# Kernel optimization log

Measured on AMD Instinct MI355X. Metric: run time of the kernel, lower is better.

## Reference

```python
import jax, jax.numpy as jnp
import numpy as np

D = 64          # feature dim
H_POS = 64      # pos_mlp hidden
H_ATTN = 4 * D  # attn_mlp hidden
B, N = 1, 1024


def setup_inputs() -> dict:
    key = jax.random.key(0)
    ks = jax.random.split(key, 12)
    s = lambda fan_in: 1.0 / np.sqrt(fan_in)
    return {
        "x": jax.random.normal(ks[0], (B, N, D), jnp.float32),
        "pos": jax.random.normal(ks[1], (B, N, 2), jnp.float32),
        "Wq": jax.random.normal(ks[2], (D, D), jnp.float32) * s(D),
        "Wk": jax.random.normal(ks[3], (D, D), jnp.float32) * s(D),
        "Wv": jax.random.normal(ks[4], (D, D), jnp.float32) * s(D),
        "pW1": jax.random.normal(ks[5], (2, H_POS), jnp.float32) * s(2),
        "pb1": jnp.zeros((H_POS,), jnp.float32),
        "pW2": jax.random.normal(ks[6], (H_POS, D), jnp.float32) * s(H_POS),
        "pb2": jnp.zeros((D,), jnp.float32),
        "aW1": jax.random.normal(ks[7], (D, H_ATTN), jnp.float32) * s(D),
        "ab1": jnp.zeros((H_ATTN,), jnp.float32),
        "aW2": jax.random.normal(ks[8], (H_ATTN, D), jnp.float32) * s(H_ATTN),
        "ab2": jnp.zeros((D,), jnp.float32),
    }


def reference(x, pos, Wq, Wk, Wv, pW1, pb1, pW2, pb2, aW1, ab1, aW2, ab2):
    # projections: [b, n, d]
    q = x @ Wq
    k = x @ Wk
    v = x @ Wv
    # pairwise relative positions: [b, i, j, 2]
    rel_pos = pos[:, :, None, :] - pos[:, None, :, :]
    # pos MLP: [b, i, j, d]
    rpe = jax.nn.relu(rel_pos @ pW1 + pb1) @ pW2 + pb2
    # pairwise q - k: [b, i, j, d]
    qk_rel = q[:, :, None, :] - k[:, None, :, :]
    # values broadcast over i, plus positional embedding: [b, i, j, d]
    vv = v[:, None, :, :] + rpe
    # attention MLP on (qk_rel + rpe): [b, i, j, d]
    sim = jax.nn.relu((qk_rel + rpe) @ aW1 + ab1) @ aW2 + ab2
    # softmax over j (axis=-2), per-channel
    attn = jax.nn.softmax(sim, axis=-2)
    # weighted aggregation: [b, i, d]
    agg = jnp.einsum('bijd,bijd->bid', attn, vv)
    return agg
```

## Files before the change

### kernel.cpp

```cpp
#include <hip/hip_runtime.h>


typedef float f32x4 __attribute__((ext_vector_type(4)));
typedef int   i32x8 __attribute__((ext_vector_type(8)));
using sh8 = __attribute__((ext_vector_type(8))) short;

static constexpr int NPTS = 1024;

#if __has_builtin(__builtin_amdgcn_exp2f)
#define EXP2(x) __builtin_amdgcn_exp2f(x)
#else
#define EXP2(x) exp2f(x)
#endif

static constexpr size_t BEXT8_OFF = 0;
static constexpr size_t AW2F_OFF = 32768;
static constexpr size_t PW2F_OFF = 49152;
static constexpr size_t CARR_OFF = 57344;
static constexpr size_t AI_OFF   = 58368;
static constexpr size_t VPT_OFF  = 320512;
static constexpr size_t AJ_OFF   = 582656;
static constexpr size_t KN8_OFF  = 713728;
static constexpr size_t QA_OFF   = 779264;

__device__ __forceinline__ unsigned short f2b_rne(float f) {
    unsigned u = __float_as_uint(f);
    u += 0x7fffu + ((u >> 16) & 1u);
    return (unsigned short)(u >> 16);
}
__device__ __forceinline__ unsigned pk2(float lo, float hi) {
    return __builtin_amdgcn_perm(__float_as_uint(hi), __float_as_uint(lo), 0x07060302);
}
__device__ __forceinline__ float b2f(unsigned short s) {
    return __uint_as_float(((unsigned)s) << 16);
}
__device__ __forceinline__ unsigned char f2fp8(float v) {
    return (unsigned char)(__builtin_amdgcn_cvt_pk_fp8_f32(v, 0.f, 0, false) & 0xff);
}
__device__ __forceinline__ unsigned pk4fp8(float a, float b, float c, float d) {
    int r = __builtin_amdgcn_cvt_pk_fp8_f32(a, b, 0, false);
    r = __builtin_amdgcn_cvt_pk_fp8_f32(c, d, r, true);
    return (unsigned)r;
}
__device__ __forceinline__ i32x8 ld32B(const void* p) {
    const uint4 a = ((const uint4*)p)[0];
    const uint4 b = ((const uint4*)p)[1];
    i32x8 r;
    r[0] = a.x; r[1] = a.y; r[2] = a.z; r[3] = a.w;
    r[4] = b.x; r[5] = b.y; r[6] = b.z; r[7] = b.w;
    return r;
}

__global__ void prep_all(const float* __restrict__ x, const float* __restrict__ pos,
                         const float* __restrict__ Wq, const float* __restrict__ Wk,
                         const float* __restrict__ Wv, const float* __restrict__ pW1,
                         const float* __restrict__ pb1, const float* __restrict__ pW2,
                         const float* __restrict__ pb2, const float* __restrict__ aW1,
                         const float* __restrict__ ab1, const float* __restrict__ aW2,
                         unsigned char* __restrict__ bext8, unsigned char* __restrict__ aw2f8,
                         unsigned short* __restrict__ pw2f, float* __restrict__ cArr,
                         unsigned char* __restrict__ kN8, float* __restrict__ vPT,
                         float* __restrict__ aI, unsigned short* __restrict__ aJ,
                         float* __restrict__ qa)
{
    __shared__ float s1[4][64];
    __shared__ float s2[4][64];
    const int b = blockIdx.x;
    if (b < 128) {
        const int r = b * 256 + threadIdx.x;
        const int frag = r >> 11, lane = (r >> 5) & 63, e = r & 31;
        const int w = frag >> 2, nt = frag & 3;
        const int tl = lane & 15, qq = lane >> 4;
        const int k = qq * 32 + e;
        const int t = 64 * w + 16 * nt + tl;
        float val;
        if (k < 64) {
            float s = 0.f;
            for (int d = 0; d < 64; ++d) s = fmaf(pW2[k * 64 + d], aW1[d * 256 + t], s);
            val = s;
        } else {
            val = aW1[(k - 64) * 256 + t];
        }
        bext8[r] = f2fp8(val);
    } else if (b < 192) {
        const int r = (b - 128) * 256 + threadIdx.x;
        const int e = r & 31, lane = (r >> 5) & 63, wsl = (r >> 11) & 3, kb = r >> 13;
        const int q = lane >> 4, dl = lane & 15;
        const int kp = kb * 128 + q * 32 + e;
        const int t = 64 * (kp >> 6) + 16 * (kp & 3) + ((kp >> 2) & 15);
        const int d = 16 * wsl + dl;
        aw2f8[r] = f2fp8(aW2[t * 64 + d] * 1.4426950408889634f);
    } else if (b < 208) {
        const int r = (b - 192) * 256 + threadIdx.x;
        const int k = r >> 6, d = r & 63;
        const int kc = k >> 5, kl = k & 31, qq = kl >> 3, e = kl & 7;
        const int nt = d >> 4, dl = d & 15;
        pw2f[(((size_t)(kc * 4 + nt) * 64) + (qq * 16 + dl)) * 8 + e] = f2b_rne(pW2[k * 64 + d]);
    } else if (b == 208) {
        const int t = threadIdx.x;
        float s = ab1[t];
        for (int d = 0; d < 64; ++d) s = fmaf(pb2[d], aW1[d * 256 + t], s);
        cArr[t] = s;
    } else if (b < 465) {
        const int t = threadIdx.x, sub = t >> 6, d = t & 63;
        const int i = (b - 209) * 4 + sub;
        s1[sub][d] = x[i * 64 + d];
        __syncthreads();
        float k = 0.f, v = 0.f;
        for (int e = 0; e < 64; ++e) {
            const float xe = s1[sub][e];
            k = fmaf(xe, Wk[e * 64 + d], k);
            v = fmaf(xe, Wv[e * 64 + d], v);
        }
        const float a = pos[i * 2] * pW1[d] + pos[i * 2 + 1] * pW1[64 + d];
        kN8[i * 64 + d] = f2fp8(-k);
        vPT[d * NPTS + i] = v + pb2[d];
        aI[i * 64 + d] = a + pb1[d];
        aJ[i * 64 + d] = f2b_rne(a);
    } else {
        const int i = b - 465, t = threadIdx.x;
        if (t < 64) s1[0][t] = x[i * 64 + t];
        __syncthreads();
        if (t < 64) {
            float s = 0.f;
            for (int e = 0; e < 64; ++e) s = fmaf(s1[0][e], Wq[e * 64 + t], s);
            s2[0][t] = s;
        }
        __syncthreads();
        float s = 0.f;
        for (int d = 0; d < 64; ++d) s = fmaf(s2[0][d], aW1[d * 256 + t], s);
        qa[(size_t)i * 256 + t] = s;
    }
}

__global__ __launch_bounds__(256, 2) void ptl_main(
    const float* __restrict__ aI, const unsigned short* __restrict__ aJ,
    const unsigned char* __restrict__ kN8, const float* __restrict__ vPT,
    const unsigned char* __restrict__ bext8, const unsigned char* __restrict__ aw2f8,
    const unsigned short* __restrict__ pw2f, const float* __restrict__ cArr,
    const float* __restrict__ qa, float* __restrict__ out)
{
    const int i    = blockIdx.x;
    const int tid  = threadIdx.x;
    const int w    = tid >> 6;
    const int lane = tid & 63;
    const int m    = lane & 15;
    const int q    = lane >> 4;

    __shared__ __align__(16) uint4 AfL[2][2][2][64];
    __shared__ __align__(16) unsigned char Af8[2][2][16 * 144];
    __shared__ __align__(16) unsigned char Hs[2][2][16 * 272];

    i32x8 B8f[4];
#pragma unroll
    for (int nt = 0; nt < 4; ++nt)
        B8f[nt] = ld32B(bext8 + ((size_t)((4 * w + nt) * 64 + lane)) * 32);
    i32x8 W2f[2];
#pragma unroll
    for (int kb = 0; kb < 2; ++kb)
        W2f[kb] = ld32B(aw2f8 + ((size_t)((kb * 4 + w) * 64 + lane)) * 32);
    sh8 P2f[2];
#pragma unroll
    for (int kc = 0; kc < 2; ++kc)
        P2f[kc] = *(const sh8*)(pw2f + ((size_t)((kc * 4 + w) * 64 + lane)) * 8);

    float creg[4];
#pragma unroll
    for (int nt = 0; nt < 4; ++nt)
        creg[nt] = cArr[64 * w + 16 * nt + m] + qa[(size_t)i * 256 + 64 * w + 16 * nt + m];

    const int s_ = w >> 1, h_ = w & 1;
    const unsigned short* bsrcA  = aJ  + m * 64 + h_ * 32 + q * 8;
    const unsigned char*  bsrcK8 = kN8 + m * 64 + h_ * 32 + q * 8;
    const float*          ibase  = aI + (size_t)i * 64 + h_ * 32 + q * 8;
    float iv[8];
    *(float4*)(iv)     = *(const float4*)(ibase);
    *(float4*)(iv + 4) = *(const float4*)(ibase + 4);

    {
        const sh8  rawA  = *(const sh8*)(bsrcA + (size_t)(16 * s_) * 64);
        const uint2 rawK = *(const uint2*)(bsrcK8 + (size_t)(16 * s_) * 64);
        float t[8];
#pragma unroll
        for (int e = 0; e < 8; ++e)
            t[e] = fmaxf(iv[e] - b2f((unsigned short)rawA[e]), 0.f);
        uint4 pk;
        pk.x = pk2(t[0], t[1]); pk.y = pk2(t[2], t[3]);
        pk.z = pk2(t[4], t[5]); pk.w = pk2(t[6], t[7]);
        AfL[0][s_][h_][lane] = pk;
        uint2 f8;
        f8.x = pk4fp8(t[0], t[1], t[2], t[3]);
        f8.y = pk4fp8(t[4], t[5], t[6], t[7]);
        *(uint2*)(Af8[0][s_] + m * 144 + h_ * 32 + q * 8)      = f8;
        *(uint2*)(Af8[0][s_] + m * 144 + 64 + h_ * 32 + q * 8) = rawK;
    }
    __syncthreads();

    float num = 0.f, den = 0.f;
    const f32x4 z4 = {0.f, 0.f, 0.f, 0.f};
    f32x4 aRp0 = z4, aRp1 = z4;
    const float* vbase = vPT + (size_t)(16 * w + m) * NPTS;

    for (int n = 0; n < 32; ++n) {
        const int pb = n & 1, nb = pb ^ 1;
        const int j0 = n << 5;

        sh8  rawA;
        uint2 rawK;
        if (n < 31) {
            rawA = *(const sh8*)(bsrcA + (size_t)(j0 + 32 + 16 * s_) * 64);
            rawK = *(const uint2*)(bsrcK8 + (size_t)(j0 + 32 + 16 * s_) * 64);
        }
        const float4 vj0 = *(const float4*)(vbase + j0 + 4 * q);
        const float4 vj1 = *(const float4*)(vbase + j0 + 16 + 4 * q);

        {
            const i32x8 A8 = ld32B(Af8[pb][0] + m * 144 + 32 * q);
            f32x4 acc[4];
#pragma unroll
            for (int nt = 0; nt < 4; ++nt) {
                const f32x4 cv = {creg[nt], creg[nt], creg[nt], creg[nt]};
                acc[nt] = __builtin_amdgcn_mfma_scale_f32_16x16x128_f8f6f4(
                    A8, B8f[nt], cv, 0, 0, 0, 127, 0, 127);
            }
            unsigned char* hw = Hs[pb][0] + (4 * q) * 272 + 64 * w + 4 * m;
#pragma unroll
            for (int r = 0; r < 4; ++r)
                *(unsigned*)(hw + r * 272) = pk4fp8(fmaxf(acc[0][r], 0.f), fmaxf(acc[1][r], 0.f),
                                                   fmaxf(acc[2][r], 0.f), fmaxf(acc[3][r], 0.f));
        }

        i32x8 h00, h01, h10, h11;
        if (n) {
            h00 = ld32B(Hs[nb][0] + m * 272 + 0   + 32 * q);
            h01 = ld32B(Hs[nb][0] + m * 272 + 128 + 32 * q);
            h10 = ld32B(Hs[nb][1] + m * 272 + 0   + 32 * q);
            h11 = ld32B(Hs[nb][1] + m * 272 + 128 + 32 * q);
        }

        {
            const i32x8 A8 = ld32B(Af8[pb][1] + m * 144 + 32 * q);
            f32x4 acc[4];
#pragma unroll
            for (int nt = 0; nt < 4; ++nt) {
                const f32x4 cv = {creg[nt], creg[nt], creg[nt], creg[nt]};
                acc[nt] = __builtin_amdgcn_mfma_scale_f32_16x16x128_f8f6f4(
                    A8, B8f[nt], cv, 0, 0, 0, 127, 0, 127);
            }
            unsigned char* hw = Hs[pb][1] + (4 * q) * 272 + 64 * w + 4 * m;
#pragma unroll
            for (int r = 0; r < 4; ++r)
                *(unsigned*)(hw + r * 272) = pk4fp8(fmaxf(acc[0][r], 0.f), fmaxf(acc[1][r], 0.f),
                                                   fmaxf(acc[2][r], 0.f), fmaxf(acc[3][r], 0.f));
        }

        const sh8 A00 = *(const sh8*)&AfL[pb][0][0][lane];
        const sh8 A01 = *(const sh8*)&AfL[pb][0][1][lane];
        const sh8 A10 = *(const sh8*)&AfL[pb][1][0][lane];
        const sh8 A11 = *(const sh8*)&AfL[pb][1][1][lane];

        if (n) {
            f32x4 aS0 = z4, aS1 = z4;
            aS0 = __builtin_amdgcn_mfma_scale_f32_16x16x128_f8f6f4(
                h00, W2f[0], aS0, 0, 0, 0, 127, 0, 127);
            aS0 = __builtin_amdgcn_mfma_scale_f32_16x16x128_f8f6f4(
                h01, W2f[1], aS0, 0, 0, 0, 127, 0, 127);
            aS1 = __builtin_amdgcn_mfma_scale_f32_16x16x128_f8f6f4(
                h10, W2f[0], aS1, 0, 0, 0, 127, 0, 127);
            aS1 = __builtin_amdgcn_mfma_scale_f32_16x16x128_f8f6f4(
                h11, W2f[1], aS1, 0, 0, 0, 127, 0, 127);
#pragma unroll
            for (int r = 0; r < 4; ++r) {
                const float e0 = EXP2(aS0[r]);
                num = fmaf(e0, aRp0[r], num);
                den += e0;
                const float e1 = EXP2(aS1[r]);
                num = fmaf(e1, aRp1[r], num);
                den += e1;
            }
        }

        const f32x4 vc0 = {vj0.x, vj0.y, vj0.z, vj0.w};
        const f32x4 vc1 = {vj1.x, vj1.y, vj1.z, vj1.w};
        f32x4 aR0 = __builtin_amdgcn_mfma_f32_16x16x32_bf16(A00, P2f[0], vc0, 0, 0, 0);
        aR0 = __builtin_amdgcn_mfma_f32_16x16x32_bf16(A01, P2f[1], aR0, 0, 0, 0);
        f32x4 aR1 = __builtin_amdgcn_mfma_f32_16x16x32_bf16(A10, P2f[0], vc1, 0, 0, 0);
        aR1 = __builtin_amdgcn_mfma_f32_16x16x32_bf16(A11, P2f[1], aR1, 0, 0, 0);
        aRp0 = aR0;
        aRp1 = aR1;

        if (n < 31) {
            float t[8];
#pragma unroll
            for (int e = 0; e < 8; ++e)
                t[e] = fmaxf(iv[e] - b2f((unsigned short)rawA[e]), 0.f);
            uint4 pk;
            pk.x = pk2(t[0], t[1]); pk.y = pk2(t[2], t[3]);
            pk.z = pk2(t[4], t[5]); pk.w = pk2(t[6], t[7]);
            AfL[nb][s_][h_][lane] = pk;
            uint2 f8;
            f8.x = pk4fp8(t[0], t[1], t[2], t[3]);
            f8.y = pk4fp8(t[4], t[5], t[6], t[7]);
            *(uint2*)(Af8[nb][s_] + m * 144 + h_ * 32 + q * 8)      = f8;
            *(uint2*)(Af8[nb][s_] + m * 144 + 64 + h_ * 32 + q * 8) = rawK;
        }

        __syncthreads();
    }

    {
        f32x4 aS0 = z4, aS1 = z4;
        const i32x8 h00 = ld32B(Hs[1][0] + m * 272 + 0   + 32 * q);
        const i32x8 h01 = ld32B(Hs[1][0] + m * 272 + 128 + 32 * q);
        const i32x8 h10 = ld32B(Hs[1][1] + m * 272 + 0   + 32 * q);
        const i32x8 h11 = ld32B(Hs[1][1] + m * 272 + 128 + 32 * q);
        aS0 = __builtin_amdgcn_mfma_scale_f32_16x16x128_f8f6f4(
            h00, W2f[0], aS0, 0, 0, 0, 127, 0, 127);
        aS0 = __builtin_amdgcn_mfma_scale_f32_16x16x128_f8f6f4(
            h01, W2f[1], aS0, 0, 0, 0, 127, 0, 127);
        aS1 = __builtin_amdgcn_mfma_scale_f32_16x16x128_f8f6f4(
            h10, W2f[0], aS1, 0, 0, 0, 127, 0, 127);
        aS1 = __builtin_amdgcn_mfma_scale_f32_16x16x128_f8f6f4(
            h11, W2f[1], aS1, 0, 0, 0, 127, 0, 127);
#pragma unroll
        for (int r = 0; r < 4; ++r) {
            const float e0 = EXP2(aS0[r]);
            num = fmaf(e0, aRp0[r], num);
            den += e0;
            const float e1 = EXP2(aS1[r]);
            num = fmaf(e1, aRp1[r], num);
            den += e1;
        }
    }

    num += __shfl_xor(num, 16);
    num += __shfl_xor(num, 32);
    den += __shfl_xor(den, 16);
    den += __shfl_xor(den, 32);
    if (q == 0) out[i * 64 + 16 * w + m] = num / den;
}

extern "C" void kernel_launch(void* const* d_in, const int* in_sizes, int n_in,
                              void* d_out, int out_size, void* d_ws, size_t ws_size,
                              hipStream_t stream) {
    const float* x   = (const float*)d_in[0];
    const float* pos = (const float*)d_in[1];
    const float* Wq  = (const float*)d_in[2];
    const float* Wk  = (const float*)d_in[3];
    const float* Wv  = (const float*)d_in[4];
    const float* pW1 = (const float*)d_in[5];
    const float* pb1 = (const float*)d_in[6];
    const float* pW2 = (const float*)d_in[7];
    const float* pb2 = (const float*)d_in[8];
    const float* aW1 = (const float*)d_in[9];
    const float* ab1 = (const float*)d_in[10];
    const float* aW2 = (const float*)d_in[11];

    char* ws = (char*)d_ws;
    unsigned char*  bext8 = (unsigned char*)(ws + BEXT8_OFF);
    unsigned char*  aw2f8 = (unsigned char*)(ws + AW2F_OFF);
    unsigned short* pw2f  = (unsigned short*)(ws + PW2F_OFF);
    float*          cArr  = (float*)(ws + CARR_OFF);
    float*          aIa   = (float*)(ws + AI_OFF);
    float*          vPTa  = (float*)(ws + VPT_OFF);
    unsigned short* aJa   = (unsigned short*)(ws + AJ_OFF);
    unsigned char*  kN8a  = (unsigned char*)(ws + KN8_OFF);
    float*          qaA   = (float*)(ws + QA_OFF);

    prep_all<<<1489, 256, 0, stream>>>(x, pos, Wq, Wk, Wv, pW1, pb1, pW2, pb2, aW1, ab1, aW2,
                                       bext8, aw2f8, pw2f, cArr, kN8a, vPTa, aIa, aJa, qaA);
    ptl_main<<<NPTS, 256, 0, stream>>>(aIa, aJa, kN8a, vPTa, bext8, aw2f8, pw2f, cArr, qaA,
                                       (float*)d_out);
}
```

Baseline: 159.7 us.

## Process 64 neighbours per pipeline step to halve barrier count

Each loop iteration now handles four 16-row j-slices (64 neighbours) instead of two, so the loop runs 16 times rather than 32. The shared-memory double buffers for A, fp8 A and hidden activations are doubled in size, and each wave builds two slices per step. This halves the number of __syncthreads barriers and gives more independent MFMA work between loads to hide latency. In exchange it raises register and LDS pressure, which could lower occupancy under launch_bounds(256,2).

Result: no change. 162.5 us (+1.7%).

```diff
diff --git a/kernel.cpp b/kernel.cpp
--- a/kernel.cpp
+++ b/kernel.cpp
@@ -147,9 +147,9 @@
     const int m    = lane & 15;
     const int q    = lane >> 4;
 
-    __shared__ __align__(16) uint4 AfL[2][2][2][64];
-    __shared__ __align__(16) unsigned char Af8[2][2][16 * 144];
-    __shared__ __align__(16) unsigned char Hs[2][2][16 * 272];
+    __shared__ __align__(16) uint4 AfL[2][4][2][64];
+    __shared__ __align__(16) unsigned char Af8[2][4][16 * 144];
+    __shared__ __align__(16) unsigned char Hs[2][4][16 * 272];
 
     i32x8 B8f[4];
 #pragma unroll
@@ -169,7 +169,7 @@
     for (int nt = 0; nt < 4; ++nt)
         creg[nt] = cArr[64 * w + 16 * nt + m] + qa[(size_t)i * 256 + 64 * w + 16 * nt + m];
 
-    const int s_ = w >> 1, h_ = w & 1;
+    const int h_ = w & 1, sA = w >> 1;
     const unsigned short* bsrcA  = aJ  + m * 64 + h_ * 32 + q * 8;
     const unsigned char*  bsrcK8 = kN8 + m * 64 + h_ * 32 + q * 8;
     const float*          ibase  = aI + (size_t)i * 64 + h_ * 32 + q * 8;
@@ -177,9 +177,7 @@
     *(float4*)(iv)     = *(const float4*)(ibase);
     *(float4*)(iv + 4) = *(const float4*)(ibase + 4);
 
-    {
-        const sh8  rawA  = *(const sh8*)(bsrcA + (size_t)(16 * s_) * 64);
-        const uint2 rawK = *(const uint2*)(bsrcK8 + (size_t)(16 * s_) * 64);
+    auto build = [&](int buf, int s, const sh8& rawA, const uint2& rawK) {
         float t[8];
 #pragma unroll
         for (int e = 0; e < 8; ++e)
@@ -187,150 +185,152 @@
         uint4 pk;
         pk.x = pk2(t[0], t[1]); pk.y = pk2(t[2], t[3]);
         pk.z = pk2(t[4], t[5]); pk.w = pk2(t[6], t[7]);
-        AfL[0][s_][h_][lane] = pk;
+        AfL[buf][s][h_][lane] = pk;
         uint2 f8;
         f8.x = pk4fp8(t[0], t[1], t[2], t[3]);
         f8.y = pk4fp8(t[4], t[5], t[6], t[7]);
-        *(uint2*)(Af8[0][s_] + m * 144 + h_ * 32 + q * 8)      = f8;
-        *(uint2*)(Af8[0][s_] + m * 144 + 64 + h_ * 32 + q * 8) = rawK;
+        *(uint2*)(Af8[buf][s] + m * 144 + h_ * 32 + q * 8)      = f8;
+        *(uint2*)(Af8[buf][s] + m * 144 + 64 + h_ * 32 + q * 8) = rawK;
+    };
+
+    auto g1pass = [&](int buf, int s) {
+        const i32x8 A8 = ld32B(Af8[buf][s] + m * 144 + 32 * q);
+        f32x4 acc[4];
+#pragma unroll
+        for (int nt = 0; nt < 4; ++nt) {
+            const f32x4 cv = {creg[nt], creg[nt], creg[nt], creg[nt]};
+            acc[nt] = __builtin_amdgcn_mfma_scale_f32_16x16x128_f8f6f4(
+                A8, B8f[nt], cv, 0, 0, 0, 127, 0, 127);
+        }
+        unsigned char* hw = Hs[buf][s] + (4 * q) * 272 + 64 * w + 4 * m;
+#pragma unroll
+        for (int r = 0; r < 4; ++r)
+            *(unsigned*)(hw + r * 272) = pk4fp8(fmaxf(acc[0][r], 0.f), fmaxf(acc[1][r], 0.f),
+                                                fmaxf(acc[2][r], 0.f), fmaxf(acc[3][r], 0.f));
+    };
+
+    {
+        const sh8  rA0 = *(const sh8*)(bsrcA + (size_t)(16 * sA) * 64);
+        const sh8  rA1 = *(const sh8*)(bsrcA + (size_t)(16 * (sA + 2)) * 64);
+        const uint2 rK0 = *(const uint2*)(bsrcK8 + (size_t)(16 * sA) * 64);
+        const uint2 rK1 = *(const uint2*)(bsrcK8 + (size_t)(16 * (sA + 2)) * 64);
+        build(0, sA, rA0, rK0);
+        build(0, sA + 2, rA1, rK1);
     }
     __syncthreads();
 
     float num = 0.f, den = 0.f;
     const f32x4 z4 = {0.f, 0.f, 0.f, 0.f};
-    f32x4 aRp0 = z4, aRp1 = z4;
+    f32x4 aRp0 = z4, aRp1 = z4, aRp2 = z4, aRp3 = z4;
     const float* vbase = vPT + (size_t)(16 * w + m) * NPTS;
 
-    for (int n = 0; n < 32; ++n) {
+    auto g2pair = [&](const i32x8& h00, const i32x8& h01, const i32x8& h10,
+                      const i32x8& h11, const f32x4& p0, const f32x4& p1) {
+        f32x4 aS0 = z4, aS1 = z4;
+        aS0 = __builtin_amdgcn_mfma_scale_f32_16x16x128_f8f6f4(h00, W2f[0], aS0, 0, 0, 0, 127, 0, 127);
+        aS0 = __builtin_amdgcn_mfma_scale_f32_16x16x128_f8f6f4(h01, W2f[1], aS0, 0, 0, 0, 127, 0, 127);
+        aS1 = __builtin_amdgcn_mfma_scale_f32_16x16x128_f8f6f4(h10, W2f[0], aS1, 0, 0, 0, 127, 0, 127);
+        aS1 = __builtin_amdgcn_mfma_scale_f32_16x16x128_f8f6f4(h11, W2f[1], aS1, 0, 0, 0, 127, 0, 127);
+#pragma unroll
+        for (int r = 0; r < 4; ++r) {
+            const float e0 = EXP2(aS0[r]);
+            num = fmaf(e0, p0[r], num);
+            den += e0;
+            const float e1 = EXP2(aS1[r]);
+            num = fmaf(e1, p1[r], num);
+            den += e1;
+        }
+    };
+
+    for (int n = 0; n < 16; ++n) {
         const int pb = n & 1, nb = pb ^ 1;
-        const int j0 = n << 5;
-
-        sh8  rawA;
-        uint2 rawK;
-        if (n < 31) {
-            rawA = *(const sh8*)(bsrcA + (size_t)(j0 + 32 + 16 * s_) * 64);
-            rawK = *(const uint2*)(bsrcK8 + (size_t)(j0 + 32 + 16 * s_) * 64);
+        const int j0 = n << 6;
+
+        sh8  rA0, rA1;
+        uint2 rK0, rK1;
+        if (n < 15) {
+            rA0 = *(const sh8*)(bsrcA + (size_t)(j0 + 64 + 16 * sA) * 64);
+            rA1 = *(const sh8*)(bsrcA + (size_t)(j0 + 64 + 16 * (sA + 2)) * 64);
+            rK0 = *(const uint2*)(bsrcK8 + (size_t)(j0 + 64 + 16 * sA) * 64);
+            rK1 = *(const uint2*)(bsrcK8 + (size_t)(j0 + 64 + 16 * (sA + 2)) * 64);
         }
         const float4 vj0 = *(const float4*)(vbase + j0 + 4 * q);
         const float4 vj1 = *(const float4*)(vbase + j0 + 16 + 4 * q);
+        const float4 vj2 = *(const float4*)(vbase + j0 + 32 + 4 * q);
+        const float4 vj3 = *(const float4*)(vbase + j0 + 48 + 4 * q);
+
+        g1pass(pb, 0);
+        g1pass(pb, 1);
+
+        i32x8 ha0, ha1, hb0, hb1;
+        if (n) {
+            ha0 = ld32B(Hs[nb][0] + m * 272 + 0   + 32 * q);
+            ha1 = ld32B(Hs[nb][0] + m * 272 + 128 + 32 * q);
+            hb0 = ld32B(Hs[nb][1] + m * 272 + 0   + 32 * q);
+            hb1 = ld32B(Hs[nb][1] + m * 272 + 128 + 32 * q);
+        }
+
+        g1pass(pb, 2);
+        g1pass(pb, 3);
+
+        if (n) g2pair(ha0, ha1, hb0, hb1, aRp0, aRp1);
+
+        if (n) {
+            const i32x8 hc0 = ld32B(Hs[nb][2] + m * 272 + 0   + 32 * q);
+            const i32x8 hc1 = ld32B(Hs[nb][2] + m * 272 + 128 + 32 * q);
+            const i32x8 hd0 = ld32B(Hs[nb][3] + m * 272 + 0   + 32 * q);
+            const i32x8 hd1 = ld32B(Hs[nb][3] + m * 272 + 128 + 32 * q);
+            g2pair(hc0, hc1, hd0, hd1, aRp2, aRp3);
+        }
 
         {
-            const i32x8 A8 = ld32B(Af8[pb][0] + m * 144 + 32 * q);
-            f32x4 acc[4];
-#pragma unroll
-            for (int nt = 0; nt < 4; ++nt) {
-                const f32x4 cv = {creg[nt], creg[nt], creg[nt], creg[nt]};
-                acc[nt] = __builtin_amdgcn_mfma_scale_f32_16x16x128_f8f6f4(
-                    A8, B8f[nt], cv, 0, 0, 0, 127, 0, 127);
-            }
-            unsigned char* hw = Hs[pb][0] + (4 * q) * 272 + 64 * w + 4 * m;
-#pragma unroll
-            for (int r = 0; r < 4; ++r)
-                *(unsigned*)(hw + r * 272) = pk4fp8(fmaxf(acc[0][r], 0.f), fmaxf(acc[1][r], 0.f),
-                                                   fmaxf(acc[2][r], 0.f), fmaxf(acc[3][r], 0.f));
-        }
-
-        i32x8 h00, h01, h10, h11;
-        if (n) {
-            h00 = ld32B(Hs[nb][0] + m * 272 + 0   + 32 * q);
-            h01 = ld32B(Hs[nb][0] + m * 272 + 128 + 32 * q);
-            h10 = ld32B(Hs[nb][1] + m * 272 + 0   + 32 * q);
-            h11 = ld32B(Hs[nb][1] + m * 272 + 128 + 32 * q);
-        }
-
+            const f32x4 vc0 = {vj0.x, vj0.y, vj0.z, vj0.w};
+            const sh8 Ak0 = *(const sh8*)&AfL[pb][0][0][lane];
+            const sh8 Ak1 = *(const sh8*)&AfL[pb][0][1][lane];
+            f32x4 aR = __builtin_amdgcn_mfma_f32_16x16x32_bf16(Ak0, P2f[0], vc0, 0, 0, 0);
+            aRp0 = __builtin_amdgcn_mfma_f32_16x16x32_bf16(Ak1, P2f[1], aR, 0, 0, 0);
+        }
         {
-            const i32x8 A8 = ld32B(Af8[pb][1] + m * 144 + 32 * q);
-            f32x4 acc[4];
-#pragma unroll
-            for (int nt = 0; nt < 4; ++nt) {
-                const f32x4 cv = {creg[nt], creg[nt], creg[nt], creg[nt]};
-                acc[nt] = __builtin_amdgcn_mfma_scale_f32_16x16x128_f8f6f4(
-                    A8, B8f[nt], cv, 0, 0, 0, 127, 0, 127);
-            }
-            unsigned char* hw = Hs[pb][1] + (4 * q) * 272 + 64 * w + 4 * m;
-#pragma unroll
-            for (int r = 0; r < 4; ++r)
-                *(unsigned*)(hw + r * 272) = pk4fp8(fmaxf(acc[0][r], 0.f), fmaxf(acc[1][r], 0.f),
-                                                   fmaxf(acc[2][r], 0.f), fmaxf(acc[3][r], 0.f));
-        }
-
-        const sh8 A00 = *(const sh8*)&AfL[pb][0][0][lane];
-        const sh8 A01 = *(const sh8*)&AfL[pb][0][1][lane];
-        const sh8 A10 = *(const sh8*)&AfL[pb][1][0][lane];
-        const sh8 A11 = *(const sh8*)&AfL[pb][1][1][lane];
-
-        if (n) {
-            f32x4 aS0 = z4, aS1 = z4;
-            aS0 = __builtin_amdgcn_mfma_scale_f32_16x16x128_f8f6f4(
-                h00, W2f[0], aS0, 0, 0, 0, 127, 0, 127);
-            aS0 = __builtin_amdgcn_mfma_scale_f32_16x16x128_f8f6f4(
-                h01, W2f[1], aS0, 0, 0, 0, 127, 0, 127);
-            aS1 = __builtin_amdgcn_mfma_scale_f32_16x16x128_f8f6f4(
-                h10, W2f[0], aS1, 0, 0, 0, 127, 0, 127);
-            aS1 = __builtin_amdgcn_mfma_scale_f32_16x16x128_f8f6f4(
-                h11, W2f[1], aS1, 0, 0, 0, 127, 0, 127);
-#pragma unroll
-            for (int r = 0; r < 4; ++r) {
-                const float e0 = EXP2(aS0[r]);
-                num = fmaf(e0, aRp0[r], num);
-                den += e0;
-                const float e1 = EXP2(aS1[r]);
-                num = fmaf(e1, aRp1[r], num);
-                den += e1;
-            }
-        }
-
-        const f32x4 vc0 = {vj0.x, vj0.y, vj0.z, vj0.w};
-        const f32x4 vc1 = {vj1.x, vj1.y, vj1.z, vj1.w};
-        f32x4 aR0 = __builtin_amdgcn_mfma_f32_16x16x32_bf16(A00, P2f[0], vc0, 0, 0, 0);
-        aR0 = __builtin_amdgcn_mfma_f32_16x16x32_bf16(A01, P2f[1], aR0, 0, 0, 0);
-        f32x4 aR1 = __builtin_amdgcn_mfma_f32_16x16x32_bf16(A10, P2f[0], vc1, 0, 0, 0);
-        aR1 = __builtin_amdgcn_mfma_f32_16x16x32_bf16(A11, P2f[1], aR1, 0, 0, 0);
-        aRp0 = aR0;
-        aRp1 = aR1;
-
-        if (n < 31) {
-            float t[8];
-#pragma unroll
-            for (int e = 0; e < 8; ++e)
-                t[e] = fmaxf(iv[e] - b2f((unsigned short)rawA[e]), 0.f);
-            uint4 pk;
-            pk.x = pk2(t[0], t[1]); pk.y = pk2(t[2], t[3]);
-            pk.z = pk2(t[4], t[5]); pk.w = pk2(t[6], t[7]);
-            AfL[nb][s_][h_][lane] = pk;
-            uint2 f8;
-            f8.x = pk4fp8(t[0], t[1], t[2], t[3]);
-            f8.y = pk4fp8(t[4], t[5], t[6], t[7]);
-            *(uint2*)(Af8[nb][s_] + m * 144 + h_ * 32 + q * 8)      = f8;
-            *(uint2*)(Af8[nb][s_] + m * 144 + 64 + h_ * 32 + q * 8) = rawK;
+            const f32x4 vc1 = {vj1.x, vj1.y, vj1.z, vj1.w};
+            const sh8 Ak0 = *(const sh8*)&AfL[pb][1][0][lane];
+            const sh8 Ak1 = *(const sh8*)&AfL[pb][1][1][lane];
+            f32x4 aR = __builtin_amdgcn_mfma_f32_16x16x32_bf16(Ak0, P2f[0], vc1, 0, 0, 0);
+            aRp1 = __builtin_amdgcn_mfma_f32_16x16x32_bf16(Ak1, P2f[1], aR, 0, 0, 0);
+        }
+        {
+            const f32x4 vc2 = {vj2.x, vj2.y, vj2.z, vj2.w};
+            const sh8 Ak0 = *(const sh8*)&AfL[pb][2][0][lane];
+            const sh8 Ak1 = *(const sh8*)&AfL[pb][2][1][lane];
+            f32x4 aR = __builtin_amdgcn_mfma_f32_16x16x32_bf16(Ak0, P2f[0], vc2, 0, 0, 0);
+            aRp2 = __builtin_amdgcn_mfma_f32_16x16x32_bf16(Ak1, P2f[1], aR, 0, 0, 0);
+        }
+        {
+            const f32x4 vc3 = {vj3.x, vj3.y, vj3.z, vj3.w};
+            const sh8 Ak0 = *(const sh8*)&AfL[pb][3][0][lane];
+            const sh8 Ak1 = *(const sh8*)&AfL[pb][3][1][lane];
+            f32x4 aR = __builtin_amdgcn_mfma_f32_16x16x32_bf16(Ak0, P2f[0], vc3, 0, 0, 0);
+            aRp3 = __builtin_amdgcn_mfma_f32_16x16x32_bf16(Ak1, P2f[1], aR, 0, 0, 0);
+        }
+
+        if (n < 15) {
+            build(nb, sA, rA0, rK0);
+            build(nb, sA + 2, rA1, rK1);
         }
 
         __syncthreads();
     }
 
     {
-        f32x4 aS0 = z4, aS1 = z4;
-        const i32x8 h00 = ld32B(Hs[1][0] + m * 272 + 0   + 32 * q);
-        const i32x8 h01 = ld32B(Hs[1][0] + m * 272 + 128 + 32 * q);
-        const i32x8 h10 = ld32B(Hs[1][1] + m * 272 + 0   + 32 * q);
-        const i32x8 h11 = ld32B(Hs[1][1] + m * 272 + 128 + 32 * q);
-        aS0 = __builtin_amdgcn_mfma_scale_f32_16x16x128_f8f6f4(
-            h00, W2f[0], aS0, 0, 0, 0, 127, 0, 127);
-        aS0 = __builtin_amdgcn_mfma_scale_f32_16x16x128_f8f6f4(
-            h01, W2f[1], aS0, 0, 0, 0, 127, 0, 127);
-        aS1 = __builtin_amdgcn_mfma_scale_f32_16x16x128_f8f6f4(
-            h10, W2f[0], aS1, 0, 0, 0, 127, 0, 127);
-        aS1 = __builtin_amdgcn_mfma_scale_f32_16x16x128_f8f6f4(
-            h11, W2f[1], aS1, 0, 0, 0, 127, 0, 127);
-#pragma unroll
-        for (int r = 0; r < 4; ++r) {
-            const float e0 = EXP2(aS0[r]);
-            num = fmaf(e0, aRp0[r], num);
-            den += e0;
-            const float e1 = EXP2(aS1[r]);
-            num = fmaf(e1, aRp1[r], num);
-            den += e1;
-        }
+        const i32x8 ha0 = ld32B(Hs[1][0] + m * 272 + 0   + 32 * q);
+        const i32x8 ha1 = ld32B(Hs[1][0] + m * 272 + 128 + 32 * q);
+        const i32x8 hb0 = ld32B(Hs[1][1] + m * 272 + 0   + 32 * q);
+        const i32x8 hb1 = ld32B(Hs[1][1] + m * 272 + 128 + 32 * q);
+        g2pair(ha0, ha1, hb0, hb1, aRp0, aRp1);
+        const i32x8 hc0 = ld32B(Hs[1][2] + m * 272 + 0   + 32 * q);
+        const i32x8 hc1 = ld32B(Hs[1][2] + m * 272 + 128 + 32 * q);
+        const i32x8 hd0 = ld32B(Hs[1][3] + m * 272 + 0   + 32 * q);
+        const i32x8 hd1 = ld32B(Hs[1][3] + m * 272 + 128 + 32 * q);
+        g2pair(hc0, hc1, hd0, hd1, aRp2, aRp3);
     }
 
     num += __shfl_xor(num, 16);
```
